# Performance work log

Hardware: AMD Instinct MI355X
Metric: run time of the kernel (lower is better)

The kernel has to match this reference:

```python
import jax, jax.numpy as jnp
import numpy as np

K = 3
STRIDE = 1
PAD = 1


def setup_inputs() -> dict:
    key = jax.random.key(0)
    k1, k2, k3 = jax.random.split(key, 3)
    N, C, H, W = 4, 256, 64, 64
    outC = 256
    x = jax.random.normal(k1, (N, C, H, W), dtype=jnp.float32)
    # offset/mask conv params (torch inits these to 0; small random makes the test nontrivial)
    conv_offset_w = jax.random.normal(k2, (3 * K * K, C, K, K), dtype=jnp.float32) * 0.01
    conv_offset_b = jnp.zeros((3 * K * K,), dtype=jnp.float32)
    # xavier-normal scale for dcn weight
    fan = C * K * K + outC * K * K
    dcn_weight = jax.random.normal(k3, (outC, C, K, K), dtype=jnp.float32) * np.float32(np.sqrt(2.0 / fan))
    return {"x": x, "conv_offset_w": conv_offset_w, "conv_offset_b": conv_offset_b, "dcn_weight": dcn_weight}


def _dcn(x, w_off, b_off, dcn_weight):
    k, s, p = K, STRIDE, PAD
    N, C, H, W = x.shape
    outC = dcn_weight.shape[0]
    KK = k * k
    # offset/mask prediction conv
    om = jax.lax.conv_general_dilated(
        x, w_off, (s, s), [(p, p), (p, p)],
        dimension_numbers=("NCHW", "OIHW", "NCHW")) + b_off[None, :, None, None]
    offset = om[:, : 2 * KK]
    mask = jax.nn.sigmoid(om[:, 2 * KK:])
    oH = (H + 2 * p - (k - 1)) // s
    oW = (W + 2 * p - (k - 1)) // s
    # pad with an extra row/col at bottom-right so floor+1 indexing is in-bounds (as in torch code)
    px = jnp.pad(x, ((0, 0), (0, 0), (p, p + 1), (p, p + 1)))
    px = jnp.transpose(px, (0, 2, 3, 1))  # (N, H+2p+1, W+2p+1, C)
    offset = jnp.transpose(offset, (0, 2, 3, 1)).reshape(N, oH, oW, KK, 2)  # (...,(y,x))
    mask = jnp.transpose(mask, (0, 2, 3, 1))  # (N, oH, oW, KK)
    base_y = jnp.arange(oH, dtype=jnp.float32) * s + p
    base_x = jnp.arange(oW, dtype=jnp.float32) * s + p
    half = (k - 1) // 2
    inner_y = jnp.repeat(jnp.arange(k, dtype=jnp.float32) - half, k)  # kernel-tap y offsets
    inner_x = jnp.tile(jnp.arange(k, dtype=jnp.float32) - half, k)   # kernel-tap x offsets
    pos_y = base_y[None, :, None, None] + inner_y[None, None, None, :] + offset[..., 0]
    pos_x = base_x[None, None, :, None] + inner_x[None, None, None, :] + offset[..., 1]
    pos_y = jnp.clip(pos_y, 0.0, H + 2 * p - 1.0)
    pos_x = jnp.clip(pos_x, 0.0, W + 2 * p - 1.0)
    y1 = jnp.floor(pos_y)
    x1 = jnp.floor(pos_x)
    y1i = y1.astype(jnp.int32)
    x1i = x1.astype(jnp.int32)
    nidx = jnp.arange(N)[:, None, None, None]
    # bilinear gathers: each (N, oH, oW, KK, C)
    v1 = px[nidx, y1i, x1i]
    v2 = px[nidx, y1i, x1i + 1]
    v3 = px[nidx, y1i + 1, x1i]
    v4 = px[nidx, y1i + 1, x1i + 1]
    lh = (pos_y - y1)[..., None]
    lw = (pos_x - x1)[..., None]
    hh = 1.0 - lh
    hw = 1.0 - lw
    value = hh * hw * v1 + hh * lw * v2 + lh * hw * v3 + lh * lw * v4
    value = value * mask[..., None]  # modulated
    w = dcn_weight.reshape(outC, C, KK)
    # sum over in_C and kernel taps -> NCHW output
    out = jnp.einsum("nhwkc,ock->nohw", value, w)
    return out


def reference(x, conv_offset_w, conv_offset_b, dcn_weight):
    return _dcn(x, conv_offset_w, conv_offset_b, dcn_weight)
```

## Files before the change

### kernel.cpp

```cpp
#include <hip/hip_runtime.h>
#include <type_traits>


typedef __bf16 bf16x8 __attribute__((ext_vector_type(8)));
typedef float  f32x4  __attribute__((ext_vector_type(4)));
typedef unsigned short ushort8 __attribute__((ext_vector_type(8)));
typedef unsigned int   uint4v  __attribute__((ext_vector_type(4)));

#define XBF_OFF   0u
#define WREP_OFF  8388608u
#define WMAIN_OFF 8536064u
#define OM_OFF    9715712u

#define LGKM0_BAR() do { __builtin_amdgcn_s_waitcnt(0xC07F); __builtin_amdgcn_s_barrier(); } while (0)

template <int N> using ic = std::integral_constant<int, N>;

__device__ __forceinline__ unsigned short f2bf(float f) {
  unsigned int u = __float_as_uint(f);
  u += 0x7fffu + ((u >> 16) & 1u);
  return (unsigned short)(u >> 16);
}
__device__ __forceinline__ float bf2f(unsigned short h) {
  return __uint_as_float(((unsigned int)h) << 16);
}

__global__ __launch_bounds__(256) void k_pre(const float* __restrict__ x,
                                             const float* __restrict__ w_off,
                                             const float* __restrict__ dcn_w,
                                             unsigned short* __restrict__ xbf,
                                             unsigned short* __restrict__ wrep,
                                             unsigned short* __restrict__ wmain) {
  __shared__ float tile[32][65];
  __shared__ unsigned short lsh[2304];
  int b = blockIdx.x;
  int t = threadIdx.x;
  if (b < 2048) {
    int n  = b >> 9;
    int cb = (b >> 6) & 7;
    int xb = b & 63;
    int xx  = t & 63;
    int cc0 = t >> 6;
#pragma unroll
    for (int j = 0; j < 8; ++j) {
      int cc = cc0 + j * 4;
      tile[cc][xx] = x[((size_t)(n * 256 + cb * 32 + cc) << 12) + xb * 64 + xx];
    }
    __syncthreads();
    int ccw = t & 31;
    int xw0 = t >> 5;
#pragma unroll
    for (int j = 0; j < 8; ++j) {
      int xw = xw0 + j * 8;
      xbf[((size_t)((n << 12) + xb * 64 + xw)) * 256 + cb * 32 + ccw] = f2bf(tile[ccw][xw]);
    }
  } else {
    int ocb = b - 2048;
    if (ocb < 32) {
      int oc = ocb;
      if (oc >= 27) {
#pragma unroll
        for (int j = 0; j < 9; ++j) wrep[oc * 2304 + j * 256 + t] = 0;
        return;
      }
      const float* base = w_off + (size_t)oc * 2304;
#pragma unroll
      for (int j = 0; j < 9; ++j) lsh[j * 256 + t] = f2bf(base[t * 9 + j]);
      __syncthreads();
#pragma unroll
      for (int j = 0; j < 9; ++j) wrep[oc * 2304 + j * 256 + t] = lsh[j * 256 + t];
    } else {
      int oc = ocb - 32;
      const float* base = dcn_w + (size_t)oc * 2304;
      int oco = ((oc >> 4) << 9) + (oc & 15) * 8;
#pragma unroll
      for (int j = 0; j < 9; ++j) {
        int k = j * 256 + t;
        wmain[((k >> 5) << 13) + oco + (((k >> 3) & 3) << 7) + (k & 7)] =
            f2bf(base[t * 9 + j]);
      }
    }
  }
}

__global__ __launch_bounds__(1024) void k_offconv(const unsigned short* __restrict__ xbf,
                                                  const unsigned short* __restrict__ wrep,
                                                  const float* __restrict__ bias,
                                                  float* __restrict__ om) {
  __shared__ __align__(16) unsigned short SHa[4][64 * 64];
  __shared__ __align__(16) unsigned short SHb[4][32 * 64];
  int t = threadIdx.x;
  int wave = t >> 6, lane = t & 63;
  int grp = wave >> 2, wv = wave & 3;
  int tg = t & 255;
  int bm = ((blockIdx.x & 7) << 5) + (blockIdx.x >> 3);
  int n = bm >> 6, oy = bm & 63;

  unsigned short* As = SHa[grp];
  unsigned short* Bs = SHb[grp];

  int arow = tg >> 2, acc4 = tg & 3;
  int brow = tg >> 3, bch = tg & 7;

  f32x4 acc0 = {0.f, 0.f, 0.f, 0.f};
  f32x4 acc1 = {0.f, 0.f, 0.f, 0.f};

  ushort8 av[2][2]; ushort8 bv[2];
  auto prefetch = [&](int ktg, auto slotc) {
    constexpr int slot = decltype(slotc)::value;
    int kk = ktg >> 2;
    int c0 = (ktg & 3) * 64;
    int dy = kk / 3 - 1, dx = kk % 3 - 1;
    int yy = oy + dy, xxg = arow + dx;
    bool ok = ((unsigned)yy < 64u) && ((unsigned)xxg < 64u);
    const unsigned short* p = xbf + (size_t)(((n * 64 + yy) * 64 + xxg) * 256 + c0 + acc4 * 16);
#pragma unroll
    for (int g = 0; g < 2; ++g)
      av[slot][g] = ok ? *(const ushort8*)(p + g * 8) : (ushort8){0,0,0,0,0,0,0,0};
    bv[slot] = *(const ushort8*)(wrep + (size_t)brow * 2304 + ktg * 64 + bch * 8);
  };

  int k0 = grp * 9;
  prefetch(k0, ic<0>{});
  prefetch(k0 + 1, ic<1>{});
  int mr = lane & 15, q = lane >> 4;

  auto step = [&](int kt, auto slotc) {
    constexpr int slot = decltype(slotc)::value;
    LGKM0_BAR();
#pragma unroll
    for (int g = 0; g < 2; ++g) {
      int ch = (acc4 * 2 + g) ^ (arow & 7);
      *(ushort8*)&As[arow * 64 + ch * 8] = av[slot][g];
    }
    { int ch = bch ^ (brow & 7);
      *(ushort8*)&Bs[brow * 64 + ch * 8] = bv[slot]; }
    if (kt + 2 < 9) prefetch(k0 + kt + 2, slotc);
    LGKM0_BAR();
#pragma unroll
    for (int kh = 0; kh < 2; ++kh) {
      int coff = ((q + kh * 4) ^ (mr & 7)) * 8;
      bf16x8 a  = *(const bf16x8*)&As[(wv * 16 + mr) * 64 + coff];
      bf16x8 b0 = *(const bf16x8*)&Bs[mr * 64 + coff];
      bf16x8 b1 = *(const bf16x8*)&Bs[(16 + mr) * 64 + coff];
      acc0 = __builtin_amdgcn_mfma_f32_16x16x32_bf16(a, b0, acc0, 0, 0, 0);
      acc1 = __builtin_amdgcn_mfma_f32_16x16x32_bf16(a, b1, acc1, 0, 0, 0);
    }
  };
  for (int kp = 0; kp < 4; ++kp) {
    step(2 * kp, ic<0>{});
    step(2 * kp + 1, ic<1>{});
  }
  step(8, ic<0>{});

  float* scratch = (float*)&SHa[0][0];
  __syncthreads();
  if (grp > 0) {
#pragma unroll
    for (int nt = 0; nt < 2; ++nt) {
      f32x4 a = nt ? acc1 : acc0;
#pragma unroll
      for (int rg = 0; rg < 4; ++rg)
        scratch[(grp - 1) * 2048 + (wv * 16 + q * 4 + rg) * 32 + nt * 16 + mr] = a[rg];
    }
  }
  __syncthreads();
  if (grp == 0) {
    int r0 = bm * 64;
#pragma unroll
    for (int nt = 0; nt < 2; ++nt) {
      f32x4 a = nt ? acc1 : acc0;
      int oc = nt * 16 + mr;
      float bvl = (oc < 27) ? bias[oc] : 0.f;
#pragma unroll
      for (int rg = 0; rg < 4; ++rg) {
        int pl = wv * 16 + q * 4 + rg;
        float v = a[rg] + bvl + scratch[pl * 32 + oc] +
                  scratch[2048 + pl * 32 + oc] + scratch[4096 + pl * 32 + oc];
        if (oc >= 18 && oc < 27) v = 1.f / (1.f + __expf(-v));
        om[(r0 + pl) * 32 + oc] = v;
      }
    }
  }
}

__global__ __launch_bounds__(1024, 4) void k_gemm_fused(const unsigned short* __restrict__ xbf,
                                                        const float* __restrict__ om,
                                                        const unsigned short* __restrict__ wB,
                                                        float* __restrict__ out) {
  __shared__ __align__(16) unsigned short Ab[2][64 * 64];
  int t = threadIdx.x;
  int wave = t >> 6, lane = t & 63;
  int bmx = ((blockIdx.x & 7) << 5) + (blockIdx.x >> 3);
  int r0 = bmx * 64;

  if (wave < 8) {
    int mr = lane & 15, q = lane >> 4;
    const unsigned short* Bg = wB + wave * 1024 + lane * 8;
    f32x4 acc[4][2];
#pragma unroll
    for (int mt = 0; mt < 4; ++mt)
#pragma unroll
      for (int nt = 0; nt < 2; ++nt) acc[mt][nt] = (f32x4){0.f, 0.f, 0.f, 0.f};

    bf16x8 bfr[2][4];

    auto citer = [&](int p, bool do_issue, bool do_mfma, auto islotc) {
      constexpr int islot = decltype(islotc)::value;
      constexpr int mslot = 1 - islot;
      if (do_issue) {
#pragma unroll
        for (int kh = 0; kh < 2; ++kh)
#pragma unroll
          for (int nt = 0; nt < 2; ++nt)
            bfr[islot][kh * 2 + nt] =
                *(const bf16x8*)(Bg + (size_t)(p * 2 + kh) * 8192 + nt * 512);
      }
      if (do_mfma) {
#pragma unroll
        for (int kh = 0; kh < 2; ++kh) {
          int coff = ((q + kh * 4) ^ (mr & 7)) * 8;
          bf16x8 af[4];
#pragma unroll
          for (int mt = 0; mt < 4; ++mt)
            af[mt] = *(const bf16x8*)&Ab[mslot][(mt * 16 + mr) * 64 + coff];
#pragma unroll
          for (int mt = 0; mt < 4; ++mt)
#pragma unroll
            for (int nt = 0; nt < 2; ++nt)
              acc[mt][nt] = __builtin_amdgcn_mfma_f32_16x16x32_bf16(
                  af[mt], bfr[mslot][kh * 2 + nt], acc[mt][nt], 0, 0, 0);
        }
      }
      LGKM0_BAR();
    };

    citer(0, true, false, ic<0>{});
    citer(1, true, true,  ic<1>{});
    for (int pp = 1; pp < 18; ++pp) {
      citer(2 * pp,     true, true, ic<0>{});
      citer(2 * pp + 1, true, true, ic<1>{});
    }
    citer(36, false, true, ic<0>{});

#pragma unroll
    for (int mt = 0; mt < 4; ++mt)
#pragma unroll
      for (int nt = 0; nt < 2; ++nt) {
        int p = r0 + mt * 16 + q * 4;
        int o = wave * 32 + nt * 16 + mr;
        int nn = p >> 12, pyx = p & 4095;
        *(f32x4*)(out + ((size_t)(nn * 256 + o) << 12) + pyx) = acc[mt][nt];
      }
  } else {
    int pt = t - 512;
    int srow = pt >> 3, sch = (pt & 7) * 8;
    int r = r0 + srow;
    int n = r >> 12, yx = r & 4095, oy = yx >> 6, ox = yx & 63;
    const unsigned short* xb = xbf + (size_t)n * (4096 * 256);
    const float* omr = om + (size_t)r * 32;
    int wchA = (((pt & 7) ^ (srow & 7)) << 3);

    float pv_y, pv_x, pv_m;
    float cw1, cw2, cw3, cw4;
    int a1, a2, a3, a4;
    float wbuf[2][4];
    ushort8 g1[2], g2[2], g3[2], g4[2];

    auto loadom = [&](int kk) {
      pv_y = omr[2 * kk]; pv_x = omr[2 * kk + 1]; pv_m = omr[18 + kk];
    };
    auto params = [&](int kk) {
      float py = (float)(oy + kk / 3) + pv_y;
      float px = (float)(ox + kk % 3) + pv_x;
      float m = pv_m;
      py = fminf(fmaxf(py, 0.f), 65.f);
      px = fminf(fmaxf(px, 0.f), 65.f);
      float fy = floorf(py), fx = floorf(px);
      float ly = py - fy, lx = px - fx;
      float hy = 1.f - ly, hx = 1.f - lx;
      int iy = (int)fy, ix = (int)fx;
      bool yv0 = (iy >= 1) && (iy <= 64);
      bool yv1 = (iy <= 63);
      bool xv0 = (ix >= 1) && (ix <= 64);
      bool xv1 = (ix <= 63);
      int y0 = min(max(iy - 1, 0), 63);
      int y1 = min(iy, 63);
      int x0 = min(max(ix - 1, 0), 63);
      int x1 = min(ix, 63);
      cw1 = (yv0 && xv0) ? hy * hx * m : 0.f;
      cw2 = (yv0 && xv1) ? hy * lx * m : 0.f;
      cw3 = (yv1 && xv0) ? ly * hx * m : 0.f;
      cw4 = (yv1 && xv1) ? ly * lx * m : 0.f;
      a1 = ((y0 << 6) + x0) * 256;
      a2 = ((y0 << 6) + x1) * 256;
      a3 = ((y1 << 6) + x0) * 256;
      a4 = ((y1 << 6) + x1) * 256;
    };

    auto issueA = [&](int ktg, auto slotc) {
      constexpr int slot = decltype(slotc)::value;
      wbuf[slot][0] = cw1; wbuf[slot][1] = cw2; wbuf[slot][2] = cw3; wbuf[slot][3] = cw4;
      int c = (ktg & 3) * 64 + sch;
      g1[slot] = *(const ushort8*)(xb + a1 + c);
      g2[slot] = *(const ushort8*)(xb + a2 + c);
      g3[slot] = *(const ushort8*)(xb + a3 + c);
      g4[slot] = *(const ushort8*)(xb + a4 + c);
    };

    loadom(0);
    params(0);
    loadom(1);
    issueA(0, ic<0>{});

    auto pphase = [&](int p, auto slotc) {
      constexpr int slot = decltype(slotc)::value;
      if (p + 1 < 36) {
        if (((p + 1) & 3) == 0) {
          int kk = (p + 1) >> 2;
          params(kk);
          loadom(kk < 8 ? kk + 1 : 8);
        }
        issueA(p + 1, ic<1 - slot>{});
      }
      uint4v rs;
#pragma unroll
      for (int pp = 0; pp < 4; ++pp) {
        float va = wbuf[slot][0] * bf2f(g1[slot][2 * pp])     + wbuf[slot][1] * bf2f(g2[slot][2 * pp]) +
                   wbuf[slot][2] * bf2f(g3[slot][2 * pp])     + wbuf[slot][3] * bf2f(g4[slot][2 * pp]);
        float vb = wbuf[slot][0] * bf2f(g1[slot][2 * pp + 1]) + wbuf[slot][1] * bf2f(g2[slot][2 * pp + 1]) +
                   wbuf[slot][2] * bf2f(g3[slot][2 * pp + 1]) + wbuf[slot][3] * bf2f(g4[slot][2 * pp + 1]);
        unsigned ua = __float_as_uint(va) + 0x8000u;
        unsigned ub = __float_as_uint(vb) + 0x8000u;
        rs[pp] = __builtin_amdgcn_perm(ub, ua, 0x07060302u);
      }
      *(uint4v*)&Ab[slot][srow * 64 + wchA] = rs;
      LGKM0_BAR();
    };

    for (int pp = 0; pp < 18; ++pp) {
      pphase(2 * pp, ic<0>{});
      pphase(2 * pp + 1, ic<1>{});
    }
    LGKM0_BAR();
  }
}

extern "C" void kernel_launch(void* const* d_in, const int* in_sizes, int n_in,
                              void* d_out, int out_size, void* d_ws, size_t ws_size,
                              hipStream_t stream) {
  const float* x     = (const float*)d_in[0];
  const float* w_off = (const float*)d_in[1];
  const float* b_off = (const float*)d_in[2];
  const float* dcn_w = (const float*)d_in[3];
  float* out = (float*)d_out;
  char* ws = (char*)d_ws;
  unsigned short* xbf   = (unsigned short*)(ws + XBF_OFF);
  unsigned short* wrep  = (unsigned short*)(ws + WREP_OFF);
  unsigned short* wmain = (unsigned short*)(ws + WMAIN_OFF);
  float*          om    = (float*)(ws + OM_OFF);

  k_pre<<<2048 + 288, 256, 0, stream>>>(x, w_off, dcn_w, xbf, wrep, wmain);
  k_offconv<<<256, 1024, 0, stream>>>(xbf, wrep, b_off, om);
  k_gemm_fused<<<256, 1024, 0, stream>>>(xbf, om, wmain, out);
}
```

Baseline: 121.2 us.

## Double the LDS tile per barrier phase and raise MFMA wave priority

```diff
diff --git a/kernel.cpp b/kernel.cpp
--- a/kernel.cpp
+++ b/kernel.cpp
@@ -188,7 +188,7 @@
                                                         const float* __restrict__ om,
                                                         const unsigned short* __restrict__ wB,
                                                         float* __restrict__ out) {
-  __shared__ __align__(16) unsigned short Ab[2][64 * 64];
+  __shared__ __align__(16) unsigned short Ab[2][64 * 128];
   int t = threadIdx.x;
   int wave = t >> 6, lane = t & 63;
   int bmx = ((blockIdx.x & 7) << 5) + (blockIdx.x >> 3);
@@ -205,43 +205,49 @@
 
     bf16x8 bfr[2][4];
 
-    auto citer = [&](int p, bool do_issue, bool do_mfma, auto islotc) {
-      constexpr int islot = decltype(islotc)::value;
-      constexpr int mslot = 1 - islot;
-      if (do_issue) {
-#pragma unroll
-        for (int kh = 0; kh < 2; ++kh)
+    auto issueB = [&](int ks, auto slotc) {
+      constexpr int slot = decltype(slotc)::value;
+#pragma unroll
+      for (int kh = 0; kh < 2; ++kh)
+#pragma unroll
+        for (int nt = 0; nt < 2; ++nt)
+          bfr[slot][kh * 2 + nt] =
+              *(const bf16x8*)(Bg + (size_t)(ks * 2 + kh) * 8192 + nt * 512);
+    };
+    auto mfma64 = [&](auto halfc, auto bufc) {
+      constexpr int half = decltype(halfc)::value;
+      constexpr int buf  = decltype(bufc)::value;
+      __builtin_amdgcn_s_setprio(1);
+#pragma unroll
+      for (int kh = 0; kh < 2; ++kh) {
+        int coff = half * 64 + ((q + kh * 4) ^ (mr & 7)) * 8;
+        bf16x8 af[4];
+#pragma unroll
+        for (int mt = 0; mt < 4; ++mt)
+          af[mt] = *(const bf16x8*)&Ab[buf][(mt * 16 + mr) * 128 + coff];
+#pragma unroll
+        for (int mt = 0; mt < 4; ++mt)
 #pragma unroll
           for (int nt = 0; nt < 2; ++nt)
-            bfr[islot][kh * 2 + nt] =
-                *(const bf16x8*)(Bg + (size_t)(p * 2 + kh) * 8192 + nt * 512);
-      }
-      if (do_mfma) {
-#pragma unroll
-        for (int kh = 0; kh < 2; ++kh) {
-          int coff = ((q + kh * 4) ^ (mr & 7)) * 8;
-          bf16x8 af[4];
-#pragma unroll
-          for (int mt = 0; mt < 4; ++mt)
-            af[mt] = *(const bf16x8*)&Ab[mslot][(mt * 16 + mr) * 64 + coff];
-#pragma unroll
-          for (int mt = 0; mt < 4; ++mt)
-#pragma unroll
-            for (int nt = 0; nt < 2; ++nt)
-              acc[mt][nt] = __builtin_amdgcn_mfma_f32_16x16x32_bf16(
-                  af[mt], bfr[mslot][kh * 2 + nt], acc[mt][nt], 0, 0, 0);
-        }
-      }
+            acc[mt][nt] = __builtin_amdgcn_mfma_f32_16x16x32_bf16(
+                af[mt], bfr[half][kh * 2 + nt], acc[mt][nt], 0, 0, 0);
+      }
+      __builtin_amdgcn_s_setprio(0);
+    };
+
+    issueB(0, ic<0>{});
+    LGKM0_BAR();
+    auto cphase = [&](int p, auto bufc) {
+      issueB(2 * p - 1, ic<1>{});
+      mfma64(ic<0>{}, bufc);
+      if (2 * p < 36) issueB(2 * p, ic<0>{});
+      mfma64(ic<1>{}, bufc);
       LGKM0_BAR();
     };
-
-    citer(0, true, false, ic<0>{});
-    citer(1, true, true,  ic<1>{});
-    for (int pp = 1; pp < 18; ++pp) {
-      citer(2 * pp,     true, true, ic<0>{});
-      citer(2 * pp + 1, true, true, ic<1>{});
-    }
-    citer(36, false, true, ic<0>{});
+    for (int pp = 0; pp < 9; ++pp) {
+      cphase(2 * pp + 1, ic<0>{});
+      cphase(2 * pp + 2, ic<1>{});
+    }
 
 #pragma unroll
     for (int mt = 0; mt < 4; ++mt)
@@ -307,22 +313,10 @@
       g3[slot] = *(const ushort8*)(xb + a3 + c);
       g4[slot] = *(const ushort8*)(xb + a4 + c);
     };
-
-    loadom(0);
-    params(0);
-    loadom(1);
-    issueA(0, ic<0>{});
-
-    auto pphase = [&](int p, auto slotc) {
+    auto blend = [&](auto slotc, auto halfc, auto bufc) {
       constexpr int slot = decltype(slotc)::value;
-      if (p + 1 < 36) {
-        if (((p + 1) & 3) == 0) {
-          int kk = (p + 1) >> 2;
-          params(kk);
-          loadom(kk < 8 ? kk + 1 : 8);
-        }
-        issueA(p + 1, ic<1 - slot>{});
-      }
+      constexpr int half = decltype(halfc)::value;
+      constexpr int buf  = decltype(bufc)::value;
       uint4v rs;
 #pragma unroll
       for (int pp = 0; pp < 4; ++pp) {
@@ -334,12 +328,37 @@
         unsigned ub = __float_as_uint(vb) + 0x8000u;
         rs[pp] = __builtin_amdgcn_perm(ub, ua, 0x07060302u);
       }
-      *(uint4v*)&Ab[slot][srow * 64 + wchA] = rs;
+      *(uint4v*)&Ab[buf][srow * 128 + half * 64 + wchA] = rs;
+    };
+
+    loadom(0);
+    params(0);
+    loadom(1);
+    issueA(0, ic<0>{});
+    issueA(1, ic<1>{});
+
+    auto pphase = [&](int p, auto bufc) {
+      blend(ic<0>{}, ic<0>{}, bufc);
+      {
+        int ksn = 2 * p + 2;
+        if (ksn < 36) {
+          if ((ksn & 3) == 0) {
+            int kk = ksn >> 2;
+            params(kk);
+            loadom(kk < 8 ? kk + 1 : 8);
+          }
+          issueA(ksn, ic<0>{});
+        }
+      }
+      blend(ic<1>{}, ic<1>{}, bufc);
+      {
+        int ksn = 2 * p + 3;
+        if (ksn < 36) issueA(ksn, ic<1>{});
+      }
       LGKM0_BAR();
     };
-
-    for (int pp = 0; pp < 18; ++pp) {
-      pphase(2 * pp, ic<0>{});
+    for (int pp = 0; pp < 9; ++pp) {
+      pphase(2 * pp,     ic<0>{});
       pphase(2 * pp + 1, ic<1>{});
     }
     LGKM0_BAR();
```

Result: faster. 114.9 us (-5.2%).
